# Performance work log

Measured on AMD Instinct MI355X. Metric: run time of the kernel, lower is better.

## Reference

```python
import jax, jax.numpy as jnp
import numpy as np


def _mlp(x, W1, b1, W2, b2, W3, b3):
    # _F: three Linear layers, each followed by ReLU (including the last one)
    x = jax.nn.relu(x @ W1 + b1)
    x = jax.nn.relu(x @ W2 + b2)
    return jax.nn.relu(x @ W3 + b3)


def setup_inputs() -> dict:
    key = jax.random.key(0)
    ks = jax.random.split(key, 11)
    B, L, E, H, O = 2, 4096, 1024, 2048, 3  # batch pinned to 2 by view((2,-1,1))
    std = jnp.float32(0.02)  # small init keeps exp(fa.fb^T) finite in fp32
    z = lambda n: jnp.zeros((n,), jnp.float32)
    return {
        "x1": jax.random.normal(ks[0], (B, L, E), jnp.float32),
        "x2": jax.random.normal(ks[1], (B, L, E), jnp.float32),
        # attend.f = _F(E, H, H)
        "fW1": jax.random.normal(ks[2], (E, H), jnp.float32) * std, "fb1": z(H),
        "fW2": jax.random.normal(ks[3], (H, H), jnp.float32) * std, "fb2": z(H),
        "fW3": jax.random.normal(ks[4], (H, H), jnp.float32) * std, "fb3": z(H),
        # compare.g = _F(E, H, H)
        "gW1": jax.random.normal(ks[5], (E, H), jnp.float32) * std, "gb1": z(H),
        "gW2": jax.random.normal(ks[6], (H, H), jnp.float32) * std, "gb2": z(H),
        "gW3": jax.random.normal(ks[7], (H, H), jnp.float32) * std, "gb3": z(H),
        # aggregate.h = _F(2H, H, O)
        "hW1": jax.random.normal(ks[8], (2 * H, H), jnp.float32) * std, "hb1": z(H),
        "hW2": jax.random.normal(ks[9], (H, H), jnp.float32) * std, "hb2": z(H),
        "hW3": jax.random.normal(ks[10], (H, O), jnp.float32) * std, "hb3": z(O),
    }


def reference(x1, x2,
              fW1, fb1, fW2, fb2, fW3, fb3,
              gW1, gb1, gW2, gb2, gW3, gb3,
              hW1, hb1, hW2, hb2, hW3, hb3):
    # ---- Attend ----
    fa = _mlp(x1, fW1, fb1, fW2, fb2, fW3, fb3)  # (B, L, H)
    fb = _mlp(x2, fW1, fb1, fW2, fb2, fW3, fb3)  # (B, L, H)
    e = jnp.exp(jnp.einsum('bih,bjh->bij', fa, fb))  # (B, L, L), exp-then-normalize as in source
    # beta[b,i] = sum_j (e[b,i,j]/sum_j e[b,i,j]) * x2[b,j]
    beta = jnp.einsum('bij,bje->bie', e / jnp.sum(e, axis=2, keepdims=True), x2)
    # alpha[b,j] = sum_i (e[b,i,j]/sum_i e[b,i,j]) * x1[b,i]
    alpha = jnp.einsum('bij,bie->bje', e / jnp.sum(e, axis=1, keepdims=True), x1)
    # ---- Compare (note: concat along SEQUENCE dim=1, faithful to the source) ----
    v1 = _mlp(jnp.concatenate([x1, beta], axis=1), gW1, gb1, gW2, gb2, gW3, gb3)   # (B, 2L, H)
    v2 = _mlp(jnp.concatenate([x2, alpha], axis=1), gW1, gb1, gW2, gb2, gW3, gb3)  # (B, 2L, H)
    # ---- Aggregate ----
    agg = jnp.concatenate([jnp.sum(v1, axis=1), jnp.sum(v2, axis=1)], axis=1)  # (B, 2H)
    out = _mlp(agg, hW1, hb1, hW2, hb2, hW3, hb3)  # (B, O)
    return out
```

## Files before the change

### kernel.cpp

```cpp
#include <hip/hip_runtime.h>
#include <hip/hip_bf16.h>
#include <cstdint>
#include <cstddef>

typedef unsigned short ushort_t;
typedef __attribute__((ext_vector_type(8))) __bf16 bf16x8;
typedef __attribute__((ext_vector_type(4))) float f32x4;
typedef __attribute__((ext_vector_type(4))) unsigned short us4;

__device__ __forceinline__ unsigned short f2bf(float f) {
    union { __hip_bfloat16 h; unsigned short u; } v;
    v.h = __float2bfloat16(f);
    return v.u;
}
__device__ __forceinline__ float bf2f(unsigned short u) {
    union { unsigned int i; float f; } v;
    v.i = ((unsigned int)u) << 16;
    return v.f;
}

__device__ __forceinline__ void gload16(const void* g, void* l) {
    __builtin_amdgcn_global_load_lds((const __attribute__((address_space(1))) void*)g,
                                     (__attribute__((address_space(3))) void*)l,
                                     16, 0, 0);
}

#define BARRIER() asm volatile("s_barrier" ::: "memory")

template<int EPI>
__global__ __launch_bounds__(512) void gemm256(
        const ushort_t* __restrict__ A, const ushort_t* __restrict__ Bt,
        ushort_t* __restrict__ C, int M, int N, int K,
        const float* __restrict__ epi_vec, float* __restrict__ rowp)
{
    __shared__ __align__(16) ushort_t lds[65536];
    __shared__ float red[2][256];
    __shared__ float rowred[4][256];

    const int nN = N >> 8;
    const int nwg = (int)gridDim.x;
    const int orig = (int)blockIdx.x;
    const int q = nwg >> 3, r = nwg & 7, xcd = orig & 7;
    const int wgid = (xcd < r ? xcd * (q + 1) : r * (q + 1) + (xcd - r) * q) + (orig >> 3);
    const int mb = wgid / nN, nb = wgid % nN;

    const int t = (int)threadIdx.x;
    const int lane = t & 63;
    const int wave = t >> 6;
    const int wm = wave >> 2;
    const int wn = wave & 3;
    const int fr = lane & 15;
    const int fk = lane >> 4;

    const int NT = K >> 6;

    const int l8 = lane >> 3;
    const int lcc = ((lane & 7) ^ (l8 & 7)) * 8;
    const ushort_t* gA = A + (size_t)(mb * 256 + wave * 8 + l8) * (size_t)K + lcc;
    const ushort_t* gB = Bt + (size_t)(nb * 256 + wave * 8 + l8) * (size_t)K + lcc;

    auto stage1 = [&](int op, int dd, int h, int j, int T2) {
        const ushort_t* g = (op ? gB : gA) + (size_t)(h * 128 + j * 64) * (size_t)K + T2 * 64;
        ushort_t* l = lds + ((op * 2 + dd) * 2 + h) * 8192 + j * 4096 + wave * 512;
        gload16(g, l);
    };
    auto stageA4 = [&](int dd, int T2) {
        stage1(0, dd, 0, 0, T2); stage1(0, dd, 0, 1, T2);
        stage1(0, dd, 1, 0, T2); stage1(0, dd, 1, 1, T2);
    };
    auto stageB4 = [&](int dd, int T2) {
        stage1(1, dd, 0, 0, T2); stage1(1, dd, 0, 1, T2);
        stage1(1, dd, 1, 0, T2); stage1(1, dd, 1, 1, T2);
    };

    const int chunk0 = ((fk) ^ (fr & 7)) * 8;
    const int chunk1 = ((4 + fk) ^ (fr & 7)) * 8;

    bf16x8 av[4], bv[4];
    auto loadA = [&](int dd, int kh, int qm) {
        const ushort_t* base = lds + ((0 * 2 + dd) * 2 + wm) * 8192;
        const int ck = kh ? chunk1 : chunk0;
#pragma unroll
        for (int mi = 0; mi < 4; ++mi)
            av[mi] = *(const bf16x8*)(base + (qm * 64 + mi * 16 + fr) * 64 + ck);
    };
    auto loadB = [&](int dd, int kh) {
        const ushort_t* base = lds + ((1 * 2 + dd) * 2 + (wn >> 1)) * 8192;
        const int ck = kh ? chunk1 : chunk0;
#pragma unroll
        for (int ni = 0; ni < 4; ++ni)
            bv[ni] = *(const bf16x8*)(base + ((wn & 1) * 64 + ni * 16 + fr) * 64 + ck);
    };

    f32x4 acc[8][4];
#pragma unroll
    for (int i = 0; i < 8; ++i)
#pragma unroll
        for (int j = 0; j < 4; ++j) acc[i][j] = f32x4{0.f, 0.f, 0.f, 0.f};

#define MM(QM) do {                                                              \
    _Pragma("unroll") for (int mi = 0; mi < 4; ++mi)                             \
    _Pragma("unroll") for (int ni = 0; ni < 4; ++ni)                             \
        acc[(QM) * 4 + mi][ni] = __builtin_amdgcn_mfma_f32_16x16x32_bf16(        \
            av[mi], bv[ni], acc[(QM) * 4 + mi][ni], 0, 0, 0);                    \
} while (0)
#define LGK_SB() do { asm volatile("s_waitcnt lgkmcnt(0)" ::: "memory");         \
                      __builtin_amdgcn_sched_barrier(0); } while (0)

    auto do_tile = [&](int T, bool stA, bool stB, int vm) {
        const int d = T & 1;
        loadB(d, 0); loadA(d, 0, 0);
        if (stA) stageA4(d ^ 1, T + 1);
        BARRIER(); LGK_SB();
        __builtin_amdgcn_s_setprio(1); MM(0); __builtin_amdgcn_s_setprio(0);
        BARRIER();
        loadA(d, 0, 1);
        BARRIER(); LGK_SB();
        __builtin_amdgcn_s_setprio(1); MM(1); __builtin_amdgcn_s_setprio(0);
        BARRIER();
        loadB(d, 1); loadA(d, 1, 0);
        BARRIER(); LGK_SB();
        __builtin_amdgcn_s_setprio(1); MM(0); __builtin_amdgcn_s_setprio(0);
        BARRIER();
        loadA(d, 1, 1);
        if (stB) stageB4(d, T + 2);
        BARRIER(); LGK_SB();
        __builtin_amdgcn_s_setprio(1); MM(1); __builtin_amdgcn_s_setprio(0);
        if (vm == 4)      asm volatile("s_waitcnt vmcnt(4)" ::: "memory");
        else if (vm == 0) asm volatile("s_waitcnt vmcnt(0)" ::: "memory");
        BARRIER();
    };

    stageA4(0, 0); stageB4(0, 0); stageB4(1, 1);
    asm volatile("s_waitcnt vmcnt(4)" ::: "memory");
    BARRIER();

    for (int T = 0; T < NT - 2; ++T) do_tile(T, true, true, 4);
    do_tile(NT - 2, true, false, 0);
    do_tile(NT - 1, false, false, -1);

#undef MM
#undef LGK_SB

    if (EPI == 0) {
#pragma unroll
        for (int mi8 = 0; mi8 < 8; ++mi8) {
            const int row0 = mb * 256 + wm * 128 + (mi8 >> 2) * 64 + (mi8 & 3) * 16 + fk * 4;
#pragma unroll
            for (int ni = 0; ni < 4; ++ni) {
                const int col = nb * 256 + wn * 64 + ni * 16 + fr;
                const float bias = epi_vec[col];
                f32x4 v = acc[mi8][ni];
#pragma unroll
                for (int j = 0; j < 4; ++j)
                    C[(size_t)(row0 + j) * N + col] = f2bf(fmaxf(v[j] + bias, 0.f));
            }
        }
    } else if (EPI == 1) {
        float rsum[8][4];
#pragma unroll
        for (int mi8 = 0; mi8 < 8; ++mi8) {
            const int row0 = mb * 256 + wm * 128 + (mi8 >> 2) * 64 + (mi8 & 3) * 16 + fk * 4;
#pragma unroll
            for (int j = 0; j < 4; ++j) rsum[mi8][j] = 0.f;
#pragma unroll
            for (int ni = 0; ni < 4; ++ni) {
                const int col = nb * 256 + wn * 64 + ni * 16 + fr;
                f32x4 v = acc[mi8][ni];
#pragma unroll
                for (int j = 0; j < 4; ++j) {
                    float x = __expf(v[j]);
                    C[(size_t)(row0 + j) * N + col] = f2bf(x);
                    rsum[mi8][j] += x;
                }
            }
        }
#pragma unroll
        for (int mi8 = 0; mi8 < 8; ++mi8)
#pragma unroll
            for (int j = 0; j < 4; ++j) {
                float s = rsum[mi8][j];
                s += __shfl_xor(s, 1); s += __shfl_xor(s, 2);
                s += __shfl_xor(s, 4); s += __shfl_xor(s, 8);
                rsum[mi8][j] = s;
            }
        if (fr == 0) {
#pragma unroll
            for (int mi8 = 0; mi8 < 8; ++mi8)
#pragma unroll
                for (int j = 0; j < 4; ++j)
                    rowred[wn][wm * 128 + (mi8 >> 2) * 64 + (mi8 & 3) * 16 + fk * 4 + j] = rsum[mi8][j];
        }
        BARRIER();
        if (t < 256)
            rowp[(size_t)nb * M + mb * 256 + t] =
                rowred[0][t] + rowred[1][t] + rowred[2][t] + rowred[3][t];
    } else {
        float cs[4] = {0.f, 0.f, 0.f, 0.f};
#pragma unroll
        for (int ni = 0; ni < 4; ++ni) {
            const int col = nb * 256 + wn * 64 + ni * 16 + fr;
            const float bias = epi_vec[col];
#pragma unroll
            for (int mi8 = 0; mi8 < 8; ++mi8) {
                f32x4 v = acc[mi8][ni];
#pragma unroll
                for (int j = 0; j < 4; ++j) cs[ni] += fmaxf(v[j] + bias, 0.f);
            }
        }
#pragma unroll
        for (int ni = 0; ni < 4; ++ni) {
            float s = cs[ni];
            s += __shfl_down(s, 32);
            s += __shfl_down(s, 16);
            cs[ni] = s;
        }
        if (fk == 0) {
#pragma unroll
            for (int ni = 0; ni < 4; ++ni) red[wm][wn * 64 + ni * 16 + fr] = cs[ni];
        }
        BARRIER();
        if (t < 256) {
            float* colpart = (float*)C;
            colpart[(size_t)mb * N + nb * 256 + t] = red[0][t] + red[1][t];
        }
    }
    asm volatile("s_waitcnt vmcnt(0)" ::: "memory");
}

template<int EPI>
__global__ __launch_bounds__(256) void gemm_bt(
        const ushort_t* __restrict__ A, const ushort_t* __restrict__ Bt,
        ushort_t* __restrict__ C, int M, int N, int K,
        const float* __restrict__ epi_vec)
{
    __shared__ __align__(16) ushort_t As[128 * 32];
    __shared__ __align__(16) ushort_t Bs[128 * 32];

    const int nN = N >> 7;
    const int nwg = (int)gridDim.x;
    const int orig = (int)blockIdx.x;
    const int q = nwg >> 3, r = nwg & 7, xcd = orig & 7;
    const int wgid = (xcd < r ? xcd * (q + 1) : r * (q + 1) + (xcd - r) * q) + (orig >> 3);
    const int mb = wgid / nN, nb = wgid % nN;

    const int t = (int)threadIdx.x;
    const int lane = t & 63;
    const int wave = t >> 6;
    const int wrow = (wave >> 1) << 6;
    const int wcol = (wave & 1) << 6;
    const int fr = lane & 15;
    const int fk = lane >> 4;

    int aoffe[4], boffe[4];
#pragma unroll
    for (int i = 0; i < 4; ++i) {
        int ra = wrow + i * 16 + fr;
        aoffe[i] = ra * 32 + (((fk ^ (ra >> 1)) & 3) << 3);
        int rb = wcol + i * 16 + fr;
        boffe[i] = rb * 32 + (((fk ^ (rb >> 1)) & 3) << 3);
    }

    const int srow = t >> 2;
    const int sslot = (t & 3) ^ ((srow >> 1) & 3);
    const ushort_t* ga = A + (size_t)(mb * 128 + srow) * K + sslot * 8;
    const ushort_t* gb = Bt + (size_t)(nb * 128 + srow) * K + sslot * 8;
    const size_t rowskip = (size_t)64 * K;
    ushort_t* lA0 = As + wave * 512;
    ushort_t* lA1 = As + 2048 + wave * 512;
    ushort_t* lB0 = Bs + wave * 512;
    ushort_t* lB1 = Bs + 2048 + wave * 512;

    f32x4 acc[4][4] = {};

    const int kiters = K >> 5;
    for (int kt = 0; kt < kiters; ++kt) {
        gload16(ga, lA0);
        gload16(ga + rowskip, lA1);
        gload16(gb, lB0);
        gload16(gb + rowskip, lB1);
        __syncthreads();
        bf16x8 af[4], bvv[4];
#pragma unroll
        for (int i = 0; i < 4; ++i) af[i] = *(const bf16x8*)(As + aoffe[i]);
#pragma unroll
        for (int i = 0; i < 4; ++i) bvv[i] = *(const bf16x8*)(Bs + boffe[i]);
#pragma unroll
        for (int mi = 0; mi < 4; ++mi)
#pragma unroll
            for (int ni = 0; ni < 4; ++ni)
                acc[mi][ni] = __builtin_amdgcn_mfma_f32_16x16x32_bf16(af[mi], bvv[ni], acc[mi][ni], 0, 0, 0);
        __syncthreads();
        ga += 32; gb += 32;
    }

#pragma unroll
    for (int mi = 0; mi < 4; ++mi) {
        const int row0 = mb * 128 + wrow + mi * 16 + fk * 4;
#pragma unroll
        for (int ni = 0; ni < 4; ++ni) {
            const int col = nb * 128 + wcol + ni * 16 + fr;
            float bias = (EPI == 0) ? epi_vec[col] : 0.f;
            f32x4 v = acc[mi][ni];
#pragma unroll
            for (int j = 0; j < 4; ++j) {
                int row = row0 + j;
                float x = v[j];
                if (EPI == 0)      x = fmaxf(x + bias, 0.f);
                else if (EPI == 1) x = __expf(x);
                else               x = x * epi_vec[row];
                C[(size_t)row * N + col] = f2bf(x);
            }
        }
    }
}

__global__ __launch_bounds__(256) void convert_x_k(const float* __restrict__ in,
                                                   ushort_t* __restrict__ out)
{
    size_t i = ((size_t)blockIdx.x * 256 + threadIdx.x) * 4;
    float4 v = *(const float4*)(in + i);
    us4 o;
    o[0] = f2bf(v.x); o[1] = f2bf(v.y); o[2] = f2bf(v.z); o[3] = f2bf(v.w);
    *(us4*)(out + i) = o;
}

__global__ void transpose_bf16_k(const ushort_t* __restrict__ in, ushort_t* __restrict__ out,
                                 int R, int C)
{
    __shared__ ushort_t tile[32][33];
    size_t bo = (size_t)blockIdx.z * R * C;
    const ushort_t* pin = in + bo;
    ushort_t* pout = out + bo;
    int c0 = blockIdx.x << 5, r0 = blockIdx.y << 5;
    int tx = threadIdx.x, ty = threadIdx.y;
#pragma unroll
    for (int i = 0; i < 4; ++i)
        tile[ty + i * 8][tx] = pin[(size_t)(r0 + ty + i * 8) * C + c0 + tx];
    __syncthreads();
#pragma unroll
    for (int i = 0; i < 4; ++i)
        pout[(size_t)(c0 + ty + i * 8) * R + r0 + tx] = tile[tx][ty + i * 8];
}

__global__ void wt_transpose_k(const float* __restrict__ in, ushort_t* __restrict__ out,
                               int R, int C)
{
    __shared__ ushort_t tile[32][33];
    int c0 = blockIdx.x << 5, r0 = blockIdx.y << 5;
    int tx = threadIdx.x, ty = threadIdx.y;
#pragma unroll
    for (int i = 0; i < 4; ++i)
        tile[ty + i * 8][tx] = f2bf(in[(size_t)(r0 + ty + i * 8) * C + c0 + tx]);
    __syncthreads();
#pragma unroll
    for (int i = 0; i < 4; ++i)
        out[(size_t)(c0 + ty + i * 8) * R + r0 + tx] = tile[tx][ty + i * 8];
}

__global__ __launch_bounds__(256) void rowrecip_k(const float* __restrict__ rowp,
                                                  float* __restrict__ out, int Mrows)
{
    int idx = blockIdx.x * 256 + threadIdx.x;
    float s = 0.f;
#pragma unroll
    for (int i = 0; i < 16; ++i) s += rowp[(size_t)i * Mrows + idx];
    out[idx] = 1.0f / s;
}

__global__ __launch_bounds__(256) void agg_reduce_k(const float* __restrict__ part,
                                                    float* __restrict__ agg)
{
    int idx = blockIdx.x * 256 + threadIdx.x;
    int g = idx >> 11, col = idx & 2047;
    int half = g >> 1, b = g & 1;
    const float* p = part + (size_t)half * 64 * 2048;
    float s = 0.f;
    for (int rr = 0; rr < 16; ++rr)
        s += p[(size_t)(b * 16 + rr) * 2048 + col] +
             p[(size_t)(32 + b * 16 + rr) * 2048 + col];
    agg[b * 4096 + half * 2048 + col] = s;
}

__global__ __launch_bounds__(256) void h_part_k(const float* __restrict__ act,
                                                const float* __restrict__ W,
                                                float* __restrict__ part, int Kdim)
{
    int j = blockIdx.x * 256 + threadIdx.x;
    int kc = blockIdx.y;
    float a0 = 0.f, a1 = 0.f;
    int k0 = kc * 16;
#pragma unroll
    for (int i = 0; i < 16; ++i) {
        int k = k0 + i;
        float w = W[(size_t)k * 2048 + j];
        a0 += act[k] * w;
        a1 += act[Kdim + k] * w;
    }
    part[(size_t)(kc * 2 + 0) * 2048 + j] = a0;
    part[(size_t)(kc * 2 + 1) * 2048 + j] = a1;
}

__global__ __launch_bounds__(256) void h_reduce_mid_k(const float* __restrict__ part,
                                                      float* __restrict__ part2)
{
    int idx = blockIdx.x * 256 + threadIdx.x;
    int g2 = idx >> 12;
    int rrow = (idx >> 11) & 1, j = idx & 2047;
    float s = 0.f;
#pragma unroll
    for (int i = 0; i < 16; ++i)
        s += part[(size_t)(((g2 * 16 + i) * 2) + rrow) * 2048 + j];
    part2[(size_t)(g2 * 2 + rrow) * 2048 + j] = s;
}

__global__ __launch_bounds__(256) void h_reduce_k(const float* __restrict__ part2,
                                                  const float* __restrict__ bias,
                                                  float* __restrict__ out, int nkc)
{
    int idx = blockIdx.x * 256 + threadIdx.x;
    int rrow = idx >> 11, j = idx & 2047;
    float s = 0.f;
    for (int kc = 0; kc < nkc; ++kc) s += part2[(size_t)(kc * 2 + rrow) * 2048 + j];
    s += bias[j];
    out[rrow * 2048 + j] = fmaxf(s, 0.f);
}

__global__ __launch_bounds__(256) void h3_k(const float* __restrict__ a2,
                                            const float* __restrict__ W,
                                            const float* __restrict__ b3,
                                            float* __restrict__ out)
{
    __shared__ float red[6][256];
    int t = threadIdx.x;
    float acc[6] = {0, 0, 0, 0, 0, 0};
    for (int k = t; k < 2048; k += 256) {
        float x0 = a2[k], x1 = a2[2048 + k];
#pragma unroll
        for (int c = 0; c < 3; ++c) {
            float w = W[k * 3 + c];
            acc[c] += x0 * w;
            acc[3 + c] += x1 * w;
        }
    }
#pragma unroll
    for (int c = 0; c < 6; ++c) red[c][t] = acc[c];
    __syncthreads();
    if (t < 6) {
        float s = 0.f;
        for (int i = 0; i < 256; ++i) s += red[t][i];
        s += b3[t < 3 ? t : t - 3];
        out[t] = fmaxf(s, 0.f);
    }
}

__global__ void diag_k(float* __restrict__ out, unsigned long long wsmb)
{
    if (threadIdx.x < 6) out[threadIdx.x] = 10000.0f + (float)wsmb;
}

constexpr size_t MB = 1024ull * 1024;
constexpr size_t OFF_W1T  = 0;
constexpr size_t OFF_W2T  = OFF_W1T  + 2048ull * 1024 * 2;
constexpr size_t OFF_W3T  = OFF_W2T  + 2048ull * 2048 * 2;
constexpr size_t OFF_XBF  = OFF_W3T  + 2048ull * 2048 * 2;
constexpr size_t OFF_R1   = OFF_XBF  + 16384ull * 1024 * 2;
constexpr size_t OFF_R2   = OFF_R1   + 64 * MB;
constexpr size_t OFF_BETA = OFF_R2   + 64 * MB;
constexpr size_t OFF_ALPHA= OFF_BETA + 2ull * 4096 * 1024 * 2;
constexpr size_t OFF_PART = OFF_ALPHA+ 2ull * 4096 * 1024 * 2;
constexpr size_t OFF_RS   = OFF_PART + 2ull * 128 * 2048 * 4;
constexpr size_t OFF_CS   = OFF_RS   + 4096 * 4;
constexpr size_t OFF_AGG  = OFF_CS   + 4096 * 4;
constexpr size_t OFF_ROWP = OFF_AGG  + 8192 * 4;
constexpr size_t OFF_END  = OFF_ROWP + 16ull * 4096 * 4;

extern "C" void kernel_launch(void* const* d_in, const int* in_sizes, int n_in,
                              void* d_out, int out_size, void* d_ws, size_t ws_size,
                              hipStream_t stream)
{
    const float* x1  = (const float*)d_in[0];
    const float* x2  = (const float*)d_in[1];
    const float* fW1 = (const float*)d_in[2];  const float* fb1 = (const float*)d_in[3];
    const float* fW2 = (const float*)d_in[4];  const float* fb2 = (const float*)d_in[5];
    const float* fW3 = (const float*)d_in[6];  const float* fb3 = (const float*)d_in[7];
    const float* gW1 = (const float*)d_in[8];  const float* gb1 = (const float*)d_in[9];
    const float* gW2 = (const float*)d_in[10]; const float* gb2 = (const float*)d_in[11];
    const float* gW3 = (const float*)d_in[12]; const float* gb3 = (const float*)d_in[13];
    const float* hW1 = (const float*)d_in[14]; const float* hb1 = (const float*)d_in[15];
    const float* hW2 = (const float*)d_in[16]; const float* hb2 = (const float*)d_in[17];
    const float* hW3 = (const float*)d_in[18]; const float* hb3 = (const float*)d_in[19];

    float* out = (float*)d_out;

    if (ws_size < OFF_END) {
        diag_k<<<1, 64, 0, stream>>>(out, (unsigned long long)(ws_size >> 20));
        return;
    }

    char* ws = (char*)d_ws;
    ushort_t* W1T  = (ushort_t*)(ws + OFF_W1T);
    ushort_t* W2T  = (ushort_t*)(ws + OFF_W2T);
    ushort_t* W3T  = (ushort_t*)(ws + OFF_W3T);
    ushort_t* XBF  = (ushort_t*)(ws + OFF_XBF);
    ushort_t* R1   = (ushort_t*)(ws + OFF_R1);
    ushort_t* R2   = (ushort_t*)(ws + OFF_R2);
    ushort_t* BETA = (ushort_t*)(ws + OFF_BETA);
    ushort_t* ALPHA= (ushort_t*)(ws + OFF_ALPHA);
    float* PART  = (float*)(ws + OFF_PART);
    float* RS    = (float*)(ws + OFF_RS);
    float* CS    = (float*)(ws + OFF_CS);
    float* AGG   = (float*)(ws + OFF_AGG);
    float* ROWP  = (float*)(ws + OFF_ROWP);

    ushort_t* PING = R2;
    ushort_t* PONG = R2 + 16777216;
    ushort_t* E    = R2;
    ushort_t* X1T  = R2 + 16777216;
    ushort_t* X2T  = R2 + 25165824;
    float* PARTH = (float*)(ws + OFF_R2);
    float* PART2 = (float*)(ws + OFF_R2 + 4 * MB);
    float* A1    = (float*)(ws + OFF_R2 + 6 * MB);
    float* A2    = (float*)(ws + OFF_R2 + 6 * MB + 16384);

    dim3 tb(32, 8);

    convert_x_k<<<8192, 256, 0, stream>>>(x1, XBF);
    convert_x_k<<<8192, 256, 0, stream>>>(x2, XBF + 8192ull * 1024);

    wt_transpose_k<<<dim3(64, 32), tb, 0, stream>>>(fW1, W1T, 1024, 2048);
    wt_transpose_k<<<dim3(64, 64), tb, 0, stream>>>(fW2, W2T, 2048, 2048);
    wt_transpose_k<<<dim3(64, 64), tb, 0, stream>>>(fW3, W3T, 2048, 2048);

    for (int c = 0; c < 2; ++c) {
        const ushort_t* src = XBF + (size_t)c * 8192 * 1024;
        ushort_t* dst = R1 + (size_t)c * 8192 * 2048;
        gemm256<0><<<256, 512, 0, stream>>>(src, W1T, PING, 8192, 2048, 1024, fb1, nullptr);
        gemm256<0><<<256, 512, 0, stream>>>(PING, W2T, PONG, 8192, 2048, 2048, fb2, nullptr);
        gemm256<0><<<256, 512, 0, stream>>>(PONG, W3T, dst, 8192, 2048, 2048, fb3, nullptr);
    }

    transpose_bf16_k<<<dim3(32, 128, 2), tb, 0, stream>>>(XBF, X1T, 4096, 1024);
    transpose_bf16_k<<<dim3(32, 128, 2), tb, 0, stream>>>(XBF + 8192ull * 1024, X2T, 4096, 1024);

    for (int b = 0; b < 2; ++b) {
        const ushort_t* fa  = R1 + (size_t)b * 4096 * 2048;
        const ushort_t* fbp = R1 + (size_t)(8192 + b * 4096) * 2048;
        gemm256<1><<<256, 512, 0, stream>>>(fa, fbp, E, 4096, 4096, 2048, nullptr, ROWP);
        rowrecip_k<<<16, 256, 0, stream>>>(ROWP, RS, 4096);
        gemm_bt<2><<<256, 256, 0, stream>>>(E, X2T + (size_t)b * 1024 * 4096,
                                            BETA + (size_t)b * 4096 * 1024,
                                            4096, 1024, 4096, RS);
        gemm256<1><<<256, 512, 0, stream>>>(fbp, fa, E, 4096, 4096, 2048, nullptr, ROWP);
        rowrecip_k<<<16, 256, 0, stream>>>(ROWP, CS, 4096);
        gemm_bt<2><<<256, 256, 0, stream>>>(E, X1T + (size_t)b * 1024 * 4096,
                                            ALPHA + (size_t)b * 4096 * 1024,
                                            4096, 1024, 4096, CS);
    }

    wt_transpose_k<<<dim3(64, 32), tb, 0, stream>>>(gW1, W1T, 1024, 2048);
    wt_transpose_k<<<dim3(64, 64), tb, 0, stream>>>(gW2, W2T, 2048, 2048);
    wt_transpose_k<<<dim3(64, 64), tb, 0, stream>>>(gW3, W3T, 2048, 2048);

    for (int c = 0; c < 2; ++c) {
        const ushort_t* xsrc = XBF + (size_t)c * 8192 * 1024;
        const ushort_t* asrc = (c == 0) ? BETA : ALPHA;
        gemm256<0><<<256, 512, 0, stream>>>(xsrc, W1T, R1, 8192, 2048, 1024, gb1, nullptr);
        gemm256<0><<<256, 512, 0, stream>>>(asrc, W1T, R1 + 8192ull * 2048, 8192, 2048, 1024, gb1, nullptr);
        gemm256<0><<<512, 512, 0, stream>>>(R1, W2T, R2, 16384, 2048, 2048, gb2, nullptr);
        gemm256<3><<<512, 512, 0, stream>>>(R2, W3T,
                                            (ushort_t*)(PART + (size_t)c * 64 * 2048),
                                            16384, 2048, 2048, gb3, nullptr);
    }
    agg_reduce_k<<<32, 256, 0, stream>>>(PART, AGG);

    h_part_k<<<dim3(8, 256), 256, 0, stream>>>(AGG, hW1, PARTH, 4096);
    h_reduce_mid_k<<<256, 256, 0, stream>>>(PARTH, PART2);
    h_reduce_k<<<16, 256, 0, stream>>>(PART2, hb1, A1, 16);
    h_part_k<<<dim3(8, 128), 256, 0, stream>>>(A1, hW2, PARTH, 2048);
    h_reduce_mid_k<<<128, 256, 0, stream>>>(PARTH, PART2);
    h_reduce_k<<<16, 256, 0, stream>>>(PART2, hb2, A2, 8);
    h3_k<<<1, 256, 0, stream>>>(A2, hW3, hb3, out);
}
```

Baseline: 1.738 ms.

## Replace barrier-heavy 4-phase GEMM tile schedule with single-sync double-buffered loop

Rewrites the GEMM main loop. The old schedule split each K-tile into four MFMA phases separated by barriers and priority changes, with staggered A/B staging. The new loop stages A and B together for the next tile and loads all LDS fragments into separate register sets so the compiler can interleave them with MFMAs. It then performs one full lgkm/vm wait plus a barrier per tile. This removes intra-tile barriers, but it holds more fragment registers and waits on global loads every tile, which may expose memory latency.

```diff
diff --git a/kernel.cpp b/kernel.cpp
--- a/kernel.cpp
+++ b/kernel.cpp
@@ -64,11 +64,9 @@
         ushort_t* l = lds + ((op * 2 + dd) * 2 + h) * 8192 + j * 4096 + wave * 512;
         gload16(g, l);
     };
-    auto stageA4 = [&](int dd, int T2) {
+    auto stageAB8 = [&](int dd, int T2) {
         stage1(0, dd, 0, 0, T2); stage1(0, dd, 0, 1, T2);
         stage1(0, dd, 1, 0, T2); stage1(0, dd, 1, 1, T2);
-    };
-    auto stageB4 = [&](int dd, int T2) {
         stage1(1, dd, 0, 0, T2); stage1(1, dd, 0, 1, T2);
         stage1(1, dd, 1, 0, T2); stage1(1, dd, 1, 1, T2);
     };
@@ -76,20 +74,19 @@
     const int chunk0 = ((fk) ^ (fr & 7)) * 8;
     const int chunk1 = ((4 + fk) ^ (fr & 7)) * 8;
 
-    bf16x8 av[4], bv[4];
-    auto loadA = [&](int dd, int kh, int qm) {
+    auto loadA4 = [&](int dd, int kh, int qm, bf16x8* dst) {
         const ushort_t* base = lds + ((0 * 2 + dd) * 2 + wm) * 8192;
         const int ck = kh ? chunk1 : chunk0;
 #pragma unroll
         for (int mi = 0; mi < 4; ++mi)
-            av[mi] = *(const bf16x8*)(base + (qm * 64 + mi * 16 + fr) * 64 + ck);
+            dst[mi] = *(const bf16x8*)(base + (qm * 64 + mi * 16 + fr) * 64 + ck);
     };
-    auto loadB = [&](int dd, int kh) {
+    auto loadB4 = [&](int dd, int kh, bf16x8* dst) {
         const ushort_t* base = lds + ((1 * 2 + dd) * 2 + (wn >> 1)) * 8192;
         const int ck = kh ? chunk1 : chunk0;
 #pragma unroll
         for (int ni = 0; ni < 4; ++ni)
-            bv[ni] = *(const bf16x8*)(base + ((wn & 1) * 64 + ni * 16 + fr) * 64 + ck);
+            dst[ni] = *(const bf16x8*)(base + ((wn & 1) * 64 + ni * 16 + fr) * 64 + ck);
     };
 
     f32x4 acc[8][4];
@@ -98,49 +95,43 @@
 #pragma unroll
         for (int j = 0; j < 4; ++j) acc[i][j] = f32x4{0.f, 0.f, 0.f, 0.f};
 
-#define MM(QM) do {                                                              \
+#define MM(QM, AV, BV) do {                                                      \
     _Pragma("unroll") for (int mi = 0; mi < 4; ++mi)                             \
     _Pragma("unroll") for (int ni = 0; ni < 4; ++ni)                             \
         acc[(QM) * 4 + mi][ni] = __builtin_amdgcn_mfma_f32_16x16x32_bf16(        \
-            av[mi], bv[ni], acc[(QM) * 4 + mi][ni], 0, 0, 0);                    \
+            AV[mi], BV[ni], acc[(QM) * 4 + mi][ni], 0, 0, 0);                    \
 } while (0)
-#define LGK_SB() do { asm volatile("s_waitcnt lgkmcnt(0)" ::: "memory");         \
-                      __builtin_amdgcn_sched_barrier(0); } while (0)
-
-    auto do_tile = [&](int T, bool stA, bool stB, int vm) {
+
+#define TILE_SYNC() do {                                                         \
+    __builtin_amdgcn_sched_barrier(0);                                           \
+    asm volatile("s_waitcnt lgkmcnt(0) vmcnt(0)" ::: "memory");                  \
+    __builtin_amdgcn_sched_barrier(0);                                           \
+    BARRIER();                                                                   \
+} while (0)
+
+    stageAB8(0, 0);
+    asm volatile("s_waitcnt vmcnt(0)" ::: "memory");
+    BARRIER();
+
+    for (int T = 0; T < NT; ++T) {
         const int d = T & 1;
-        loadB(d, 0); loadA(d, 0, 0);
-        if (stA) stageA4(d ^ 1, T + 1);
-        BARRIER(); LGK_SB();
-        __builtin_amdgcn_s_setprio(1); MM(0); __builtin_amdgcn_s_setprio(0);
-        BARRIER();
-        loadA(d, 0, 1);
-        BARRIER(); LGK_SB();
-        __builtin_amdgcn_s_setprio(1); MM(1); __builtin_amdgcn_s_setprio(0);
-        BARRIER();
-        loadB(d, 1); loadA(d, 1, 0);
-        BARRIER(); LGK_SB();
-        __builtin_amdgcn_s_setprio(1); MM(0); __builtin_amdgcn_s_setprio(0);
-        BARRIER();
-        loadA(d, 1, 1);
-        if (stB) stageB4(d, T + 2);
-        BARRIER(); LGK_SB();
-        __builtin_amdgcn_s_setprio(1); MM(1); __builtin_amdgcn_s_setprio(0);
-        if (vm == 4)      asm volatile("s_waitcnt vmcnt(4)" ::: "memory");
-        else if (vm == 0) asm volatile("s_waitcnt vmcnt(0)" ::: "memory");
-        BARRIER();
-    };
-
-    stageA4(0, 0); stageB4(0, 0); stageB4(1, 1);
-    asm volatile("s_waitcnt vmcnt(4)" ::: "memory");
-    BARRIER();
-
-    for (int T = 0; T < NT - 2; ++T) do_tile(T, true, true, 4);
-    do_tile(NT - 2, true, false, 0);
-    do_tile(NT - 1, false, false, -1);
+        bf16x8 a0[4], a1[4], a2[4], a3[4], b0[4], b1[4];
+        loadB4(d, 0, b0);
+        loadA4(d, 0, 0, a0);
+        if (T + 1 < NT) stageAB8(d ^ 1, T + 1);
+        loadA4(d, 0, 1, a1);
+        MM(0, a0, b0);
+        loadB4(d, 1, b1);
+        loadA4(d, 1, 0, a2);
+        MM(1, a1, b0);
+        loadA4(d, 1, 1, a3);
+        MM(0, a2, b1);
+        MM(1, a3, b1);
+        TILE_SYNC();
+    }
 
 #undef MM
-#undef LGK_SB
+#undef TILE_SYNC
 
     if (EPI == 0) {
 #pragma unroll
```

Result: faster. 1.614 ms (-7.1%).
